# Kernel tuning notes

Measured on AMD Instinct MI355X. Metric: run time of the kernel, lower is better.

## Reference

```python
import jax, jax.numpy as jnp
import numpy as np
from jax import lax

DN = ('NDHWC', 'DHWIO', 'NDHWC')
SHAPE = (33, 33, 33)
B = 2
N = 40000
C = 64


def setup_inputs() -> dict:
    key = jax.random.key(0)
    ks = jax.random.split(key, 24)
    D, H, W = SHAPE
    # unique active voxel coords (batch, z, y, x)
    rng = np.random.default_rng(0)
    idx = rng.choice(B * D * H * W, size=N, replace=False)
    b = idx // (D * H * W)
    r = idx % (D * H * W)
    coors = np.stack([b, r // (H * W), (r // W) % H, r % W], axis=1).astype(np.int32)

    def w(k, shape, scale=0.1):
        return jax.random.normal(k, shape, jnp.float32) * scale

    inp = {
        'features': jax.random.normal(ks[0], (N, 3), jnp.float32),
        'coors': jnp.asarray(coors),
        'batch_size': B,
        'w1': w(ks[1], (3, 3, 3, 3, C), 0.2), 'b1': w(ks[2], (C,), 0.05),
        'w2': w(ks[3], (3, 3, 3, C, C), 0.05), 'b2': w(ks[4], (C,), 0.05),
        'w3': w(ks[5], (3, 3, 3, C, C), 0.05), 'b3': w(ks[6], (C,), 0.05),
        'wt': w(ks[7], (3, 3, 3, C, C), 0.05), 'bt': w(ks[8], (C,), 0.05),
        'w5': w(ks[9], (3, 3, 3, C, C), 0.05), 'b5': w(ks[10], (C,), 0.05),
    }
    # folded eval-mode BatchNorm: y = x*s + h  (s = gamma/sqrt(var+eps), h = beta - mean*s)
    for i, (sk, hk) in enumerate(zip(ks[11:16], ks[16:21]), start=1):
        inp[f's{i}'] = 1.0 + 0.1 * jax.random.normal(sk, (C,), jnp.float32)
        inp[f'h{i}'] = 0.05 * jax.random.normal(hk, (C,), jnp.float32)
    return inp


def _forward(features, coors, batch_size,
             w1, b1, w2, b2, w3, b3, wt, bt, w5, b5,
             s1, h1, s2, h2, s3, h3, s4, h4, s5, h5):
    D, H, W = SHAPE
    bi, zi, yi, xi = coors[:, 0], coors[:, 1], coors[:, 2], coors[:, 3]
    # densify SparseConvTensor (zeros at inactive sites) + active mask
    x = jnp.zeros((batch_size, D, H, W, features.shape[-1]), features.dtype)
    x = x.at[bi, zi, yi, xi].set(features)
    m = jnp.zeros((batch_size, D, H, W, 1), jnp.float32).at[bi, zi, yi, xi].set(1.0)
    ones3 = jnp.ones((3, 3, 3, 1, 1), jnp.float32)

    conv = lambda a, k, pad: lax.conv_general_dilated(a, k, (1, 1, 1), pad, dimension_numbers=DN)
    # masked BN(eval) + ReLU: applied only on active sites, background stays exactly 0
    act = lambda y, mm, s, h: jnp.where(mm, jax.nn.relu(y * s + h), 0.0)

    # SparseConv3d(3,64,3): valid conv; output actives = 1-dilation of input actives
    x = conv(x, w1, 'VALID')
    m1 = conv(m, ones3, 'VALID') > 0  # [B,31,31,31,1]
    x = act(x + b1, m1, s1, h1)

    # two SubMConv3d(64,64,3) sharing indice_key: same active set, SAME padding
    x = act(conv(x, w2, 'SAME') + b2, m1, s2, h2)
    x = act(conv(x, w3, 'SAME') + b3, m1, s3, h3)

    # SparseConvTranspose3d(64,64,3,2): out = (D-1)*2+3; actives = transposed dilation
    x = lax.conv_transpose(x, wt, (2, 2, 2), 'VALID', dimension_numbers=DN)
    mT = lax.conv_transpose(m1.astype(jnp.float32), ones3, (2, 2, 2), 'VALID', dimension_numbers=DN) > 0
    x = act(x + bt, mT, s4, h4)

    # ToDense -> dense Conv3d(64,64,3) -> BN -> ReLU (dense: applied everywhere)
    x = conv(x, w5, 'VALID') + b5
    x = jax.nn.relu(x * s5 + h5)
    return jnp.transpose(x, (0, 4, 1, 2, 3))  # NCDHW like spconv ToDense output


def reference(features, coors, batch_size,
              w1, b1, w2, b2, w3, b3, wt, bt, w5, b5,
              s1, h1, s2, h2, s3, h3, s4, h4, s5, h5):
    return _forward(features, coors, batch_size,
                    w1, b1, w2, b2, w3, b3, wt, bt, w5, b5,
                    s1, h1, s2, h2, s3, h3, s4, h4, s5, h5)
```

## Files before the change

kernel.cpp:

```cpp
#include <hip/hip_runtime.h>
#include <cstdint>

constexpr int BB = 2, C = 64;
constexpr int D1 = 31;
constexpr int DP = 33;
constexpr int D4 = 63;
constexpr int D5 = 61;
constexpr int D5CUBE = D5*D5*D5;

constexpr int NV1 = BB*D1*D1*D1;
constexpr int NVP = BB*DP*DP*DP;
constexpr int NV4 = BB*D4*D4*D4;
constexpr int NV5 = BB*D5*D5*D5;

constexpr size_t alup(size_t x) { return (x + 255) & ~(size_t)255; }
constexpr size_t OB_X0  = 0;
constexpr size_t OB_M0  = alup(OB_X0  + (size_t)NVP*3*4);
constexpr size_t OB_M1P = alup(OB_M0  + (size_t)NVP*4);
constexpr size_t OB_X1  = alup(OB_M1P + (size_t)NVP*4);
constexpr size_t OB_X2  = alup(OB_X1  + (size_t)NVP*64*2);
constexpr size_t OB_X3  = alup(OB_X2  + (size_t)NVP*64*2);
constexpr size_t OB_MT  = alup(OB_X3  + (size_t)NVP*64*2);
constexpr size_t OB_X4  = alup(OB_MT  + (size_t)NV4*4);
constexpr size_t OB_WB2 = alup(OB_X4  + (size_t)NV4*64*2);
constexpr size_t OB_WB3 = alup(OB_WB2 + (size_t)27*64*64*2);
constexpr size_t OB_WBT = alup(OB_WB3 + (size_t)27*64*64*2);
constexpr size_t OB_WB5 = alup(OB_WBT + (size_t)27*64*64*2);

typedef __attribute__((ext_vector_type(8))) short short8;
typedef __attribute__((ext_vector_type(4))) float f32x4;

__device__ inline unsigned short f2bf(float f) {
  unsigned int u = __float_as_uint(f);
  u = (u + 0x7FFFu + ((u >> 16) & 1u)) >> 16;
  return (unsigned short)u;
}

template<int DD>
__device__ inline void decodev(int vox, int& b, int& z, int& y, int& x) {
  x = vox % DD; int r = vox / DD;
  y = r % DD;   r /= DD;
  z = r % DD;   b = r / DD;
}

__device__ inline int xcd_swz(int bid, int nb) {
  int q = nb >> 3, r = nb & 7;
  int xcd = bid & 7, idx = bid >> 3;
  return (xcd < r ? xcd*(q+1) : r*(q+1) + (xcd - r)*q) + idx;
}

__global__ void __launch_bounds__(256)
k_zero(float* __restrict__ x0, float* __restrict__ m0, float* __restrict__ m1p,
       unsigned short* __restrict__ x1, unsigned short* __restrict__ x2,
       unsigned short* __restrict__ x3) {
  int v = blockIdx.x*256 + threadIdx.x;
  if (v >= NVP) return;
  m0[v] = 0.f; m1p[v] = 0.f;
  x0[3*v+0] = 0.f; x0[3*v+1] = 0.f; x0[3*v+2] = 0.f;
  int x = v % DP, r = v / DP;
  int y = r % DP; r /= DP;
  int z = r % DP;
  if (x==0 || x==DP-1 || y==0 || y==DP-1 || z==0 || z==DP-1) {
    ulonglong2 zz = {0ull, 0ull};
    ulonglong2* p1 = (ulonglong2*)(x1 + (size_t)v*64);
    ulonglong2* p2 = (ulonglong2*)(x2 + (size_t)v*64);
    ulonglong2* p3 = (ulonglong2*)(x3 + (size_t)v*64);
    #pragma unroll
    for (int i = 0; i < 8; i++) { p1[i] = zz; p2[i] = zz; p3[i] = zz; }
  }
}

__global__ void k_scatter(const float* __restrict__ feat, const int* __restrict__ coors,
                          int n, float* __restrict__ x0, float* __restrict__ m0) {
  int i = blockIdx.x*blockDim.x + threadIdx.x;
  if (i >= n) return;
  int b = coors[4*i+0], z = coors[4*i+1], y = coors[4*i+2], x = coors[4*i+3];
  int v = ((b*DP + z)*DP + y)*DP + x;
  x0[v*3+0] = feat[3*i+0];
  x0[v*3+1] = feat[3*i+1];
  x0[v*3+2] = feat[3*i+2];
  m0[v] = 1.0f;
}

__global__ void __launch_bounds__(256)
k_conv1(const float* __restrict__ x0, const float* __restrict__ m0,
        unsigned short* __restrict__ x1, float* __restrict__ m1p,
        const float* __restrict__ w1, const float* __restrict__ b1,
        const float* __restrict__ s1, const float* __restrict__ h1) {
  long long t = (long long)blockIdx.x*blockDim.x + threadIdx.x;
  if (t >= (long long)NV1*C) return;
  int co  = (int)(t & 63);
  int vox = (int)(t >> 6);
  int b, z, y, x; decodev<D1>(vox, b, z, y, x);
  float sum = 0.f, mm = 0.f;
  #pragma unroll
  for (int kz=0; kz<3; kz++)
  #pragma unroll
  for (int ky=0; ky<3; ky++)
  #pragma unroll
  for (int kx=0; kx<3; kx++) {
    int iv = ((b*DP + z+kz)*DP + y+ky)*DP + (x+kx);
    mm += m0[iv];
    const float* px = x0 + iv*3;
    const float* pw = w1 + ((kz*3+ky)*3+kx)*3*64 + co;
    sum += px[0]*pw[0] + px[1]*pw[64] + px[2]*pw[128];
  }
  bool m = mm > 0.f;
  float o = m ? fmaxf((sum + b1[co])*s1[co] + h1[co], 0.f) : 0.f;
  size_t pOff = (size_t)(((b*DP + z+1)*DP + y+1)*DP + (x+1));
  x1[pOff*C + co] = f2bf(o);
  if (co == 0) m1p[pOff] = m ? 1.f : 0.f;
}

__global__ void k_repack4(const float* __restrict__ wa, const float* __restrict__ wb,
                          const float* __restrict__ wc, const float* __restrict__ wd,
                          unsigned short* __restrict__ da, unsigned short* __restrict__ db,
                          unsigned short* __restrict__ dc, unsigned short* __restrict__ dd) {
  int which = blockIdx.x / 432;
  int i = (blockIdx.x - which*432)*256 + threadIdx.x;
  const float* w = which == 0 ? wa : which == 1 ? wb : which == 2 ? wc : wd;
  unsigned short* dst = which == 0 ? da : which == 1 ? db : which == 2 ? dc : dd;
  int co = i & 63, k = (i >> 6) & 63, t = i >> 12;
  int kk = k >> 5, q = (k >> 3) & 3, j = k & 7, cb = co >> 4, l = q*16 + (co & 15);
  dst[(size_t)((t*2+kk)*4+cb)*512 + l*8 + j] = f2bf(w[i]);
}

__global__ void __launch_bounds__(256)
k_maskT(const float* __restrict__ m1p, float* __restrict__ mt) {
  int vox = blockIdx.x*256 + threadIdx.x;
  if (vox >= NV4) return;
  int b, zo, yo, xo; decodev<D4>(vox, b, zo, yo, xo);
  float mm = 0.f;
  for (int kz = 0; kz < 3; kz++) {
    if ((zo + kz) & 1) continue;
    int izp = ((zo + kz - 2) >> 1) + 1;
    for (int ky = 0; ky < 3; ky++) {
      if ((yo + ky) & 1) continue;
      int iyp = ((yo + ky - 2) >> 1) + 1;
      for (int kx = 0; kx < 3; kx++) {
        if ((xo + kx) & 1) continue;
        int ixp = ((xo + kx - 2) >> 1) + 1;
        mm += m1p[((b*DP + izp)*DP + iyp)*DP + ixp];
      }
    }
  }
  mt[vox] = mm;
}

__device__ __forceinline__ void c_step2(const short8 (&A)[2], const short8 (&W)[4],
                                        f32x4 (&acc)[2][4]) {
  #pragma unroll
  for (int a = 0; a < 2; a++)
    #pragma unroll
    for (int cb = 0; cb < 4; cb++)
      acc[a][cb] = __builtin_amdgcn_mfma_f32_16x16x32_bf16(W[cb], A[a], acc[a][cb], 0, 0, 0);
}

constexpr int C23_HALF = 1280;

__global__ void __launch_bounds__(256)
k_conv23_mfma(const unsigned short* __restrict__ xin, const unsigned short* __restrict__ wB,
              unsigned short* __restrict__ xout, const float* __restrict__ m1p,
              const float* __restrict__ bias, const float* __restrict__ s,
              const float* __restrict__ h) {
  __shared__ short8 sA[2*C23_HALF];
  const int tid  = threadIdx.x;
  const int lane = tid & 63;
  const int wid  = tid >> 6;
  const int ll   = lane & 15;
  const int l16  = lane >> 4;

  const int blk = xcd_swz(blockIdx.x, gridDim.x);
  const int yt  = blk & 7;
  const int rzb = blk >> 3;
  const int z   = rzb % D1;
  const int b   = rzb / D1;
  const int y0  = yt * 4;

  int st_r[5], st_base[5];
  #pragma unroll
  for (int it = 0; it < 5; ++it) {
    int g = it*256 + tid; g = g > 1055 ? 1055 : g;
    int r = g / 264, rem = g - r*264;
    int v = rem >> 3, c16p = rem & 7;
    int c16l = c16p ^ (v & 7);
    st_r[it] = r;
    st_base[it] = (v << 7) + (c16l << 4);
  }

  const char* xinb = (const char*)xin;

  f32x4 acc[2][4];
  #pragma unroll
  for (int a = 0; a < 2; a++)
    #pragma unroll
    for (int cb = 0; cb < 4; cb++)
      acc[a][cb] = f32x4{0.f, 0.f, 0.f, 0.f};

  auto STAGE = [&](int kzn, int kyn, int hn) {
    size_t pb = (size_t)((b*DP + z + kzn)*DP) * (DP*128);
    char* dst = (char*)&sA[0] + hn*(C23_HALF*16);
    #pragma unroll
    for (int it = 0; it < 5; ++it) {
      int yin = y0 + st_r[it] + kyn; yin = yin > 32 ? 32 : yin;
      __builtin_amdgcn_global_load_lds(
        (const __attribute__((address_space(1))) void*)(xinb + pb + (size_t)yin*(DP*128) + st_base[it]),
        (__attribute__((address_space(3))) void*)(dst + it*4096 + wid*1024),
        16, 0, 0);
    }
  };
  auto LDA = [&](int hh, int kx, int kk, short8 (&A)[2]) {
    #pragma unroll
    for (int a = 0; a < 2; a++) {
      int xv = a*16 + ll; xv = xv > 30 ? 30 : xv;
      int v  = xv + kx;
      int ch = hh*C23_HALF + wid*264 + v*8 + ((kk*4 + l16) ^ (v & 7));
      A[a] = sA[ch];
    }
  };

  short8 A0[2], A1[2];

  STAGE(0, 0, 0);
  __syncthreads();

  int kzn = 0, kyn = 1;
  #pragma unroll 1
  for (int p = 0; p < 9; ++p) {
    const int hh = p & 1;

    short8 W[6][4];
    {
      const unsigned short* wp = wB + (size_t)p*12288 + lane*8;
      #pragma unroll
      for (int st = 0; st < 6; ++st)
        #pragma unroll
        for (int cb = 0; cb < 4; cb++)
          W[st][cb] = *reinterpret_cast<const short8*>(wp + st*2048 + cb*512);
    }
    __builtin_amdgcn_sched_barrier(0);

    if (p < 8) {
      STAGE(kzn, kyn, hh ^ 1);
      kyn++; if (kyn == 3) { kyn = 0; kzn++; }
    }
    __builtin_amdgcn_sched_barrier(0);

    LDA(hh, 0, 0, A0);
    #pragma unroll
    for (int st = 0; st < 6; ++st) {
      const int kxn = (st+1) >> 1, kkn = (st+1) & 1;
      if (st < 5) {
        if (st & 1) LDA(hh, kxn, kkn, A0); else LDA(hh, kxn, kkn, A1);
      }
      if (st & 1) c_step2(A1, W[st], acc); else c_step2(A0, W[st], acc);
    }
    __syncthreads();
  }

  const int y = y0 + wid;
  if (y < D1) {
    #pragma unroll
    for (int a = 0; a < 2; a++) {
      int x = a*16 + ll;
      if (x >= D1) continue;
      size_t pOff = (size_t)(((b*DP + z+1)*DP + y+1)*DP + (x+1));
      bool m = m1p[pOff] > 0.f;
      #pragma unroll
      for (int cb = 0; cb < 4; cb++) {
        unsigned long long pack = 0;
        #pragma unroll
        for (int r = 0; r < 4; r++) {
          int co = cb*16 + l16*4 + r;
          float o = m ? fmaxf((acc[a][cb][r] + bias[co])*s[co] + h[co], 0.f) : 0.f;
          pack |= (unsigned long long)f2bf(o) << (16*r);
        }
        *reinterpret_cast<unsigned long long*>(xout + pOff*64 + cb*16 + l16*4) = pack;
      }
    }
  }
}

constexpr int CT_CHUNKS = 1792;

__global__ void __launch_bounds__(256)
k_convT_mfma(const unsigned short* __restrict__ x3, const unsigned short* __restrict__ wB,
             unsigned short* __restrict__ x4, const float* __restrict__ mt,
             const float* __restrict__ bias, const float* __restrict__ s,
             const float* __restrict__ h) {
  __shared__ short8 sb[CT_CHUNKS];
  const int tid  = threadIdx.x;
  const int lane = tid & 63;
  const int wid  = tid >> 6;
  const int ii   = lane & 15;
  const int l16  = lane >> 4;

  const int blk   = xcd_swz(blockIdx.x, gridDim.x);
  const int ytile = blk & 15;
  const int rzb   = blk >> 4;
  const int zo    = rzb % D4;
  const int b     = rzb / D4;
  const int y0    = ytile * 4;

  const int izp0 = (zo + (zo & 1)) >> 1;
  const int izp1 = (zo & 1) ? izp0 : izp0 + 1;

  #pragma unroll
  for (int it = 0; it < 7; ++it) {
    int g = it*256 + tid; g = g > 1583 ? 1583 : g;
    int r6 = g / 264, rem = g - r6*264;
    int v = rem >> 3, c16p = rem & 7;
    int c16l = c16p ^ (v & 7);
    int pz  = r6 >= 3 ? 1 : 0;
    int ry  = r6 - pz*3;
    int izp = pz ? izp1 : izp0;
    int iyp = ytile*2 + ry;
    size_t srcB = ((size_t)((b*DP + izp)*DP + iyp)*DP)*128 + (size_t)(v << 7) + (c16l << 4);
    __builtin_amdgcn_global_load_lds(
      (const __attribute__((address_space(1))) void*)((const char*)x3 + srcB),
      (__attribute__((address_space(3))) void*)((char*)&sb[0] + it*4096 + wid*1024),
      16, 0, 0);
  }
  __syncthreads();

  f32x4 acc[4][4];
  #pragma unroll
  for (int a = 0; a < 4; a++)
    #pragma unroll
    for (int cb = 0; cb < 4; cb++)
      acc[a][cb] = f32x4{0.f, 0.f, 0.f, 0.f};

  const int yo = y0 + wid;
  if (yo < D4) {
    const int nPz = (zo & 1) ? 1 : 2;
    #pragma unroll 1
    for (int pz = 0; pz < 2; ++pz) {
      if (pz >= nPz) break;
      const int kz = (zo & 1) ? 1 : pz*2;
      #pragma unroll 1
      for (int kyi = 0; kyi < 2; ++kyi) {
        int ky, ry;
        if (wid & 1) { if (kyi == 1) break; ky = 1; ry = (wid + 1) >> 1; }
        else         { ky = kyi*2;          ry = (wid >> 1) + kyi; }
        const int rbase = (pz*3 + ry)*264;
        #pragma unroll
        for (int kx = 0; kx < 3; ++kx) {
          const int apar  = kx & 1;
          const int xoffE = ((kx + apar - 2) >> 1) + 1;
          const int t = (kz*3 + ky)*3 + kx;
          #pragma unroll
          for (int kk = 0; kk < 2; ++kk) {
            short8 Bv[4];
            const unsigned short* wpk = wB + (size_t)(t*2+kk)*2048 + lane*8;
            #pragma unroll
            for (int cb = 0; cb < 4; cb++)
              Bv[cb] = *reinterpret_cast<const short8*>(wpk + cb*512);
            #pragma unroll
            for (int ablk = 0; ablk < 2; ablk++) {
              const int ixp = ablk*16 + ii + xoffE;
              short8 A = sb[rbase + ixp*8 + ((kk*4 + l16) ^ (ixp & 7))];
              const int afr = apar*2 + ablk;
              #pragma unroll
              for (int cb = 0; cb < 4; cb++)
                acc[afr][cb] = __builtin_amdgcn_mfma_f32_16x16x32_bf16(A, Bv[cb], acc[afr][cb], 0, 0, 0);
            }
          }
        }
      }
    }

    float bv[4], sv[4], hv[4];
    #pragma unroll
    for (int cb = 0; cb < 4; cb++) {
      int c = cb*16 + (lane & 15);
      bv[cb] = bias[c]; sv[cb] = s[c]; hv[cb] = h[c];
    }
    const int rowBase = ((b*D4 + zo)*D4 + yo)*D4;
    #pragma unroll
    for (int a = 0; a < 4; a++) {
      const int ablk = a & 1, apar = a >> 1;
      #pragma unroll
      for (int r = 0; r < 4; r++) {
        const int row = (lane >> 4)*4 + r;
        const int xo  = 2*(ablk*16 + row) + apar;
        if (xo >= D4) continue;
        const int vox = rowBase + xo;
        const bool m = mt[vox] > 0.f;
        #pragma unroll
        for (int cb = 0; cb < 4; cb++) {
          float o = m ? fmaxf((acc[a][cb][r] + bv[cb])*sv[cb] + hv[cb], 0.f) : 0.f;
          x4[(size_t)vox*64 + cb*16 + (lane & 15)] = f2bf(o);
        }
      }
    }
  }
}

__global__ void __launch_bounds__(256)
k_conv5_mfma(const unsigned short* __restrict__ x4, const unsigned short* __restrict__ wB,
             float* __restrict__ out, const float* __restrict__ bias,
             const float* __restrict__ s, const float* __restrict__ h) {
  __shared__ short8 sA[2][1280];
  const int tid  = threadIdx.x;
  const int lane = tid & 63;
  const int wid  = tid >> 6;
  const int ll   = lane & 15;
  const int l16  = lane >> 4;

  const int blk = xcd_swz(blockIdx.x, gridDim.x);
  const int xt  = blk & 1;
  const int yt  = (blk >> 1) & 15;
  const int rzb = blk >> 5;
  const int z   = rzb % D5;
  const int b   = rzb / D5;
  const int y0  = yt * 4;
  const int xbase = xt * 32;

  int st_off[5];
  #pragma unroll
  for (int it = 0; it < 5; ++it) {
    int g = it*64 + lane;
    int v = g >> 3, c16p = g & 7;
    int c16l = c16p ^ (v & 7);
    st_off[it] = xt*4096 + (v << 7) + (c16l << 4);
  }

  const char* x4b = (const char*)x4;

  f32x4 acc[2][4];
  #pragma unroll
  for (int a = 0; a < 2; a++)
    #pragma unroll
    for (int cb = 0; cb < 4; cb++)
      acc[a][cb] = f32x4{0.f, 0.f, 0.f, 0.f};

  auto STAGE = [&](int kzn, int kyn, int hn) {
    int yin = y0 + wid + kyn; yin = yin > 62 ? 62 : yin;
    size_t rb = ((size_t)((b*D4 + z + kzn)*D4 + yin)) * 8064;
    char* dst = (char*)&sA[hn][0] + wid*5120;
    #pragma unroll
    for (int it = 0; it < 5; ++it) {
      __builtin_amdgcn_global_load_lds(
        (const __attribute__((address_space(1))) void*)(x4b + rb + st_off[it]),
        (__attribute__((address_space(3))) void*)(dst + it*1024),
        16, 0, 0);
    }
  };
  auto LDA = [&](int hh, int kx, int kk, short8 (&A)[2]) {
    #pragma unroll
    for (int a = 0; a < 2; a++) {
      int v = a*16 + ll + kx;
      int ch = hh*1280 + wid*320 + v*8 + ((kk*4 + l16) ^ (v & 7));
      A[a] = sA[0][ch];
    }
  };

  short8 A0[2], A1[2];

  STAGE(0, 0, 0);
  __syncthreads();

  int kzn = 0, kyn = 1;
  #pragma unroll 1
  for (int p = 0; p < 9; ++p) {
    const int hh = p & 1;

    short8 W[6][4];
    {
      const unsigned short* wp = wB + (size_t)p*12288 + lane*8;
      #pragma unroll
      for (int st = 0; st < 6; ++st)
        #pragma unroll
        for (int cb = 0; cb < 4; cb++)
          W[st][cb] = *reinterpret_cast<const short8*>(wp + st*2048 + cb*512);
    }
    __builtin_amdgcn_sched_barrier(0);

    if (p < 8) {
      STAGE(kzn, kyn, hh ^ 1);
      kyn++; if (kyn == 3) { kyn = 0; kzn++; }
    }
    __builtin_amdgcn_sched_barrier(0);

    LDA(hh, 0, 0, A0);
    #pragma unroll
    for (int st = 0; st < 6; ++st) {
      const int kxn = (st+1) >> 1, kkn = (st+1) & 1;
      if (st < 5) {
        if (st & 1) LDA(hh, kxn, kkn, A0); else LDA(hh, kxn, kkn, A1);
      }
      if (st & 1) c_step2(A1, W[st], acc); else c_step2(A0, W[st], acc);
    }
    __syncthreads();
  }

  const int yout = y0 + wid;
  if (yout < D5) {
    #pragma unroll
    for (int a = 0; a < 2; a++) {
      int x = xbase + a*16 + ll;
      if (x >= D5) continue;
      size_t sp = (size_t)(z*D5 + yout)*D5 + x;
      #pragma unroll
      for (int cb = 0; cb < 4; cb++)
        #pragma unroll
        for (int r = 0; r < 4; r++) {
          int co = cb*16 + l16*4 + r;
          float o = fmaxf((acc[a][cb][r] + bias[co])*s[co] + h[co], 0.f);
          out[(size_t)(b*64 + co)*D5CUBE + sp] = o;
        }
    }
  }
}

extern "C" void kernel_launch(void* const* d_in, const int* in_sizes, int n_in,
                              void* d_out, int out_size, void* d_ws, size_t ws_size,
                              hipStream_t stream) {
  const float* feat  = (const float*)d_in[0];
  const int*   coors = (const int*)d_in[1];
  const float* w1 = (const float*)d_in[3];
  const float* b1 = (const float*)d_in[4];
  const float* w2 = (const float*)d_in[5];
  const float* b2 = (const float*)d_in[6];
  const float* w3 = (const float*)d_in[7];
  const float* b3 = (const float*)d_in[8];
  const float* wt = (const float*)d_in[9];
  const float* bt = (const float*)d_in[10];
  const float* w5 = (const float*)d_in[11];
  const float* b5 = (const float*)d_in[12];
  const float* s1 = (const float*)d_in[13];
  const float* h1 = (const float*)d_in[14];
  const float* s2 = (const float*)d_in[15];
  const float* h2 = (const float*)d_in[16];
  const float* s3 = (const float*)d_in[17];
  const float* h3 = (const float*)d_in[18];
  const float* s4 = (const float*)d_in[19];
  const float* h4 = (const float*)d_in[20];
  const float* s5 = (const float*)d_in[21];
  const float* h5 = (const float*)d_in[22];
  int n = in_sizes[0] / 3;

  char* wsb = (char*)d_ws;
  float*          X0  = (float*)(wsb + OB_X0);
  float*          M0  = (float*)(wsb + OB_M0);
  float*          M1P = (float*)(wsb + OB_M1P);
  unsigned short* X1  = (unsigned short*)(wsb + OB_X1);
  unsigned short* X2  = (unsigned short*)(wsb + OB_X2);
  unsigned short* X3  = (unsigned short*)(wsb + OB_X3);
  float*          MT  = (float*)(wsb + OB_MT);
  unsigned short* X4  = (unsigned short*)(wsb + OB_X4);
  unsigned short* WB2 = (unsigned short*)(wsb + OB_WB2);
  unsigned short* WB3 = (unsigned short*)(wsb + OB_WB3);
  unsigned short* WBT = (unsigned short*)(wsb + OB_WBT);
  unsigned short* WB5 = (unsigned short*)(wsb + OB_WB5);

  k_zero<<<(NVP + 255)/256, 256, 0, stream>>>(X0, M0, M1P, X1, X2, X3);

  k_repack4<<<1728, 256, 0, stream>>>(w2, w3, wt, w5, WB2, WB3, WBT, WB5);

  k_scatter<<<(n+255)/256, 256, 0, stream>>>(feat, coors, n, X0, M0);

  {
    long long threads = (long long)NV1*C;
    k_conv1<<<(int)((threads+255)/256), 256, 0, stream>>>(X0, M0, X1, M1P, w1, b1, s1, h1);
  }

  constexpr int BLK23 = BB * D1 * 8;
  k_conv23_mfma<<<BLK23, 256, 0, stream>>>(X1, WB2, X2, M1P, b2, s2, h2);
  k_conv23_mfma<<<BLK23, 256, 0, stream>>>(X2, WB3, X3, M1P, b3, s3, h3);

  k_maskT<<<(NV4 + 255)/256, 256, 0, stream>>>(M1P, MT);

  constexpr int BLK_T = BB * D4 * 16;
  k_convT_mfma<<<BLK_T, 256, 0, stream>>>(X3, WBT, X4, MT, bt, s4, h4);

  constexpr int BLK5 = BB * D5 * 16 * 2;
  k_conv5_mfma<<<BLK5, 256, 0, stream>>>(X4, WB5, (float*)d_out, b5, s5, h5);
}
```

Measured before the change: 355.9 us.

## Widen conv5 tile to full 64-wide x rows and stagger MFMA order per wave

The dense conv5 kernel now has each block cover a full 61-wide x row (4 x-subtiles per wave) instead of splitting x into two halves. This halves the block count and removes the duplicated staging of overlapping input rows and weight loads per block. The staging loop is redistributed across all 256 threads, and odd waves process the weight slices in a rotated order to spread LDS access. LDS use grows and so does accumulator register pressure (16 f32x4 accumulators plus three A buffers), so launch_bounds(256,2) is added, which may cap occupancy or cause spills.

```diff
diff --git a/kernel.cpp b/kernel.cpp
--- a/kernel.cpp
+++ b/kernel.cpp
@@ -151,6 +151,15 @@
                                         f32x4 (&acc)[2][4]) {
   #pragma unroll
   for (int a = 0; a < 2; a++)
+    #pragma unroll
+    for (int cb = 0; cb < 4; cb++)
+      acc[a][cb] = __builtin_amdgcn_mfma_f32_16x16x32_bf16(W[cb], A[a], acc[a][cb], 0, 0, 0);
+}
+
+__device__ __forceinline__ void c5_step(const short8 (&A)[4], const short8 (&W)[4],
+                                        f32x4 (&acc)[4][4]) {
+  #pragma unroll
+  for (int a = 0; a < 4; a++)
     #pragma unroll
     for (int cb = 0; cb < 4; cb++)
       acc[a][cb] = __builtin_amdgcn_mfma_f32_16x16x32_bf16(W[cb], A[a], acc[a][cb], 0, 0, 0);
@@ -396,69 +405,81 @@
   }
 }
 
-__global__ void __launch_bounds__(256)
+__global__ void __launch_bounds__(256, 2)
 k_conv5_mfma(const unsigned short* __restrict__ x4, const unsigned short* __restrict__ wB,
              float* __restrict__ out, const float* __restrict__ bias,
              const float* __restrict__ s, const float* __restrict__ h) {
-  __shared__ short8 sA[2][1280];
+  __shared__ short8 sA[2][2048];
   const int tid  = threadIdx.x;
   const int lane = tid & 63;
   const int wid  = tid >> 6;
   const int ll   = lane & 15;
   const int l16  = lane >> 4;
 
-  const int blk = xcd_swz(blockIdx.x, gridDim.x);
-  const int xt  = blk & 1;
-  const int yt  = (blk >> 1) & 15;
-  const int rzb = blk >> 5;
-  const int z   = rzb % D5;
-  const int b   = rzb / D5;
-  const int y0  = yt * 4;
-  const int xbase = xt * 32;
-
-  int st_off[5];
-  #pragma unroll
-  for (int it = 0; it < 5; ++it) {
-    int g = it*64 + lane;
-    int v = g >> 3, c16p = g & 7;
+  const int blk   = xcd_swz(blockIdx.x, gridDim.x);
+  const int ytile = blk & 15;
+  const int rzb   = blk >> 4;
+  const int z     = rzb % D5;
+  const int b     = rzb / D5;
+  const int y0    = ytile * 4;
+
+  int st_r[8], st_base[8];
+  #pragma unroll
+  for (int it = 0; it < 8; ++it) {
+    int g = it*256 + tid; g = g > 2015 ? 2015 : g;
+    int r = g / 504, rem = g - r*504;
+    int v = rem >> 3, c16p = rem & 7;
     int c16l = c16p ^ (v & 7);
-    st_off[it] = xt*4096 + (v << 7) + (c16l << 4);
+    st_r[it] = r;
+    st_base[it] = (v << 7) + (c16l << 4);
   }
 
   const char* x4b = (const char*)x4;
 
-  f32x4 acc[2][4];
-  #pragma unroll
-  for (int a = 0; a < 2; a++)
+  f32x4 acc[4][4];
+  #pragma unroll
+  for (int a = 0; a < 4; a++)
     #pragma unroll
     for (int cb = 0; cb < 4; cb++)
       acc[a][cb] = f32x4{0.f, 0.f, 0.f, 0.f};
 
-  auto STAGE = [&](int kzn, int kyn, int hn) {
-    int yin = y0 + wid + kyn; yin = yin > 62 ? 62 : yin;
-    size_t rb = ((size_t)((b*D4 + z + kzn)*D4 + yin)) * 8064;
-    char* dst = (char*)&sA[hn][0] + wid*5120;
-    #pragma unroll
-    for (int it = 0; it < 5; ++it) {
+  auto STAGE_A = [&](int kzn, int kyn, int hn) {
+    size_t pb = (size_t)(b*D4 + z + kzn) * (D4*D4*128);
+    char* dst = (char*)&sA[hn][0];
+    #pragma unroll
+    for (int it = 0; it < 8; ++it) {
+      int yin = y0 + st_r[it] + kyn; yin = yin > 62 ? 62 : yin;
       __builtin_amdgcn_global_load_lds(
-        (const __attribute__((address_space(1))) void*)(x4b + rb + st_off[it]),
-        (__attribute__((address_space(3))) void*)(dst + it*1024),
+        (const __attribute__((address_space(1))) void*)(x4b + pb + (size_t)yin*8064 + st_base[it]),
+        (__attribute__((address_space(3))) void*)(dst + it*4096 + wid*1024),
         16, 0, 0);
     }
   };
-  auto LDA = [&](int hh, int kx, int kk, short8 (&A)[2]) {
-    #pragma unroll
-    for (int a = 0; a < 2; a++) {
-      int v = a*16 + ll + kx;
-      int ch = hh*1280 + wid*320 + v*8 + ((kk*4 + l16) ^ (v & 7));
-      A[a] = sA[0][ch];
+  auto LDA = [&](int hh, int kx, int kk, short8 (&A)[4]) {
+    #pragma unroll
+    for (int a = 0; a < 4; a++) {
+      int v  = a*16 + ll + kx;
+      int ch = wid*504 + v*8 + ((kk*4 + l16) ^ (v & 7));
+      A[a] = sA[hh][ch];
     }
   };
 
-  short8 A0[2], A1[2];
-
-  STAGE(0, 0, 0);
+  short8 A0[4], A1[4], A2[4];
+
+  STAGE_A(0, 0, 0);
   __syncthreads();
+
+#define C5_BODY(p0,p1,p2,p3,p4,p5)                                    \
+  do {                                                                 \
+    LDA(hh, (p0)>>1, (p0)&1, A0);                                      \
+    LDA(hh, (p1)>>1, (p1)&1, A1);                                      \
+    LDA(hh, (p2)>>1, (p2)&1, A2);  c5_step(A0, W[p0], acc);            \
+    LDA(hh, (p3)>>1, (p3)&1, A0);  c5_step(A1, W[p1], acc);            \
+    LDA(hh, (p4)>>1, (p4)&1, A1);  c5_step(A2, W[p2], acc);            \
+    LDA(hh, (p5)>>1, (p5)&1, A2);  c5_step(A0, W[p3], acc);            \
+    c5_step(A1, W[p4], acc);                                           \
+    c5_step(A2, W[p5], acc);                                           \
+  } while (0)
 
   int kzn = 0, kyn = 1;
   #pragma unroll 1
@@ -477,28 +498,25 @@
     __builtin_amdgcn_sched_barrier(0);
 
     if (p < 8) {
-      STAGE(kzn, kyn, hh ^ 1);
+      STAGE_A(kzn, kyn, hh ^ 1);
       kyn++; if (kyn == 3) { kyn = 0; kzn++; }
     }
     __builtin_amdgcn_sched_barrier(0);
 
-    LDA(hh, 0, 0, A0);
-    #pragma unroll
-    for (int st = 0; st < 6; ++st) {
-      const int kxn = (st+1) >> 1, kkn = (st+1) & 1;
-      if (st < 5) {
-        if (st & 1) LDA(hh, kxn, kkn, A0); else LDA(hh, kxn, kkn, A1);
-      }
-      if (st & 1) c_step2(A1, W[st], acc); else c_step2(A0, W[st], acc);
+    if ((wid & 1) == 0) {
+      C5_BODY(0,1,2,3,4,5);
+    } else {
+      C5_BODY(3,4,5,0,1,2);
     }
     __syncthreads();
   }
+#undef C5_BODY
 
   const int yout = y0 + wid;
   if (yout < D5) {
     #pragma unroll
-    for (int a = 0; a < 2; a++) {
-      int x = xbase + a*16 + ll;
+    for (int a = 0; a < 4; a++) {
+      int x = a*16 + ll;
       if (x >= D5) continue;
       size_t sp = (size_t)(z*D5 + yout)*D5 + x;
       #pragma unroll
@@ -574,6 +592,6 @@
   constexpr int BLK_T = BB * D4 * 16;
   k_convT_mfma<<<BLK_T, 256, 0, stream>>>(X3, WBT, X4, MT, bt, s4, h4);
 
-  constexpr int BLK5 = BB * D5 * 16 * 2;
+  constexpr int BLK5 = BB * D5 * 16;
   k_conv5_mfma<<<BLK5, 256, 0, stream>>>(X4, WB5, (float*)d_out, b5, s5, h5);
 }
```

Measured after the change: 321.2 us. -9.8%, faster.
